# Optimization experiments

Hardware: AMD Instinct MI355X
Metric: run time of the kernel (lower is better)

The kernel has to match this reference:

```python
import jax, jax.numpy as jnp
import numpy as np

B, K, D, H = 4, 2048, 768, 12
HD = D // H
NEG = -1e30  # stands in for -inf in the additive mask


def setup_inputs() -> dict:
    key = jax.random.key(0)
    ks = jax.random.split(key, 11)
    s = 1.0 / np.sqrt(D)
    inp = {
        "x": jax.random.normal(ks[0], (B, K, D), jnp.float32),
        "is_context": jax.random.randint(ks[1], (B, K), 0, 2) > 0,
        "Wq": jax.random.normal(ks[2], (D, D), jnp.float32) * s,
        "bq": jax.random.normal(ks[3], (D,), jnp.float32) * 0.01,
        "Wk": jax.random.normal(ks[4], (D, D), jnp.float32) * s,
        "bk": jax.random.normal(ks[5], (D,), jnp.float32) * 0.01,
        "Wv": jax.random.normal(ks[6], (D, D), jnp.float32) * s,
        "bv": jax.random.normal(ks[7], (D,), jnp.float32) * 0.01,
        "Wo": jax.random.normal(ks[8], (D, D), jnp.float32) * s,
        "bo": jax.random.normal(ks[9], (D,), jnp.float32) * 0.01,
    }
    return inp


def reference(x, is_context, Wq, bq, Wk, bk, Wv, bv, Wo, bo):
    b, k_len, d = x.shape
    scale = 1.0 / jnp.sqrt(jnp.asarray(HD, x.dtype))
    # torch nn.Linear: y = x @ W.T + b
    q = (x @ Wq.T + bq).reshape(b, k_len, H, HD).transpose(0, 2, 1, 3)  # [B,H,K,hd]
    kk = (x @ Wk.T + bk).reshape(b, k_len, H, HD).transpose(0, 2, 1, 3)
    v = (x @ Wv.T + bv).reshape(b, k_len, H, HD).transpose(0, 2, 1, 3)

    ctx = is_context  # [B,K] bool
    # allowed[b,i,j]: context rows attend only to context cols; target rows attend to all
    allowed = (ctx[:, :, None] & ctx[:, None, :]) | (~ctx)[:, :, None]  # [B,K,K]

    scores = jnp.einsum("bhqd,bhkd->bhqk", q, kk) * scale  # [B,H,K,K]
    scores = jnp.where(allowed[:, None, :, :], scores, NEG)
    attn = jax.nn.softmax(scores, axis=-1)
    out = jnp.einsum("bhqk,bhkd->bhqd", attn, v)  # [B,H,K,hd]
    out = out.transpose(0, 2, 1, 3).reshape(b, k_len, d)
    return out @ Wo.T + bo
```

## Files before the change

### kernel.cpp

```cpp
#include <hip/hip_runtime.h>
#include <hip/hip_bf16.h>

constexpr int BATCH = 4;
constexpr int SEQ   = 2048;
constexpr int DIM   = 768;
constexpr int NH    = 12;
constexpr int HDIM  = 64;

typedef __attribute__((ext_vector_type(8))) short bf16x8;
typedef __attribute__((ext_vector_type(4))) float f32x4;
typedef __attribute__((ext_vector_type(4))) short s16x4;

__device__ inline short f2bf(float f) {
    union { float f; unsigned u; } v; v.f = f;
    unsigned r = (v.u + 0x7fff + ((v.u >> 16) & 1)) >> 16;
    return (short)r;
}

__device__ inline unsigned pack_bf16x2(float a, float b) {
    union { __hip_bfloat162 h; unsigned u; } c;
    c.h = __float22bfloat162_rn(make_float2(a, b));
    return c.u;
}

__device__ inline float fast_exp2(float x) {
#if __has_builtin(__builtin_amdgcn_exp2f)
    return __builtin_amdgcn_exp2f(x);
#else
    return __expf(x * 0.6931471805599453f);
#endif
}

__device__ inline void gld16(const short* g, short* l) {
    __builtin_amdgcn_global_load_lds(
        (const __attribute__((address_space(1))) void*)g,
        (__attribute__((address_space(3))) void*)l, 16, 0, 0);
}

__device__ inline bool ctx_at(const void* p, bool isU8, int idx) {
    return isU8 ? (((const unsigned char*)p)[idx] != 0)
                : (((const int*)p)[idx] != 0);
}

__global__ __launch_bounds__(256) void prep_kernel(
    const float* __restrict__ x,  const float* __restrict__ Wq,
    const float* __restrict__ Wk, const float* __restrict__ Wv,
    const float* __restrict__ Wo,
    short* __restrict__ xb,  short* __restrict__ Wqb,
    short* __restrict__ Wkb, short* __restrict__ Wvb,
    short* __restrict__ Wob,
    const unsigned char* __restrict__ ctxm, int ctxbytes, int* __restrict__ flag) {
    const int blk = blockIdx.x;
    constexpr int XBLK = (BATCH * SEQ * DIM / 4) / 256;
    constexpr int WBLK = (DIM * DIM / 4) / 256;

    if (blk == XBLK + 4 * WBLK) {
        __shared__ int cnt;
        if (threadIdx.x == 0) cnt = 0;
        __syncthreads();
        int local = 0;
        for (int i = threadIdx.x; i < ctxbytes; i += 256)
            if ((i & 3) != 0 && ctxm[i] != 0) local++;
        atomicAdd(&cnt, local);
        __syncthreads();
        if (threadIdx.x == 0) *flag = (cnt > 0) ? 1 : 0;
        return;
    }

    const float* src; short* dst; int i;
    if (blk < XBLK) {
        src = x; dst = xb;
        i = blk * 256 + threadIdx.x;
    } else {
        const int r = blk - XBLK;
        const int w = r / WBLK;
        src = (w == 0) ? Wq : (w == 1) ? Wk : (w == 2) ? Wv : Wo;
        dst = (w == 0) ? Wqb : (w == 1) ? Wkb : (w == 2) ? Wvb : Wob;
        i = (r - w * WBLK) * 256 + threadIdx.x;
    }
    float4 v = ((const float4*)src)[i];
    s16x4 o;
    o.x = f2bf(v.x); o.y = f2bf(v.y); o.z = f2bf(v.z); o.w = f2bf(v.w);
    ((s16x4*)dst)[i] = o;
}

template <bool BF16OUT>
__global__ __launch_bounds__(256) void gemm_mfma(
    const short* __restrict__ A,
    const short* __restrict__ W0, const float* __restrict__ bias0, void* __restrict__ C0,
    const short* __restrict__ W1, const float* __restrict__ bias1, void* __restrict__ C1,
    const short* __restrict__ W2, const float* __restrict__ bias2, void* __restrict__ C2,
    float scale0) {
    constexpr int N  = DIM;
    constexpr int Kd = DIM;

    const short* W; const float* bias; void* C; float scale;
    if (blockIdx.z == 0)      { W = W0; bias = bias0; C = C0; scale = scale0; }
    else if (blockIdx.z == 1) { W = W1; bias = bias1; C = C1; scale = 1.f; }
    else                      { W = W2; bias = bias2; C = C2; scale = 1.f; }

    const int tid  = threadIdx.x;
    const int wave = tid >> 6;
    const int lane = tid & 63;
    const int quad = lane >> 4;
    const int l16  = lane & 15;
    const int wm   = wave & 1;
    const int wn   = wave >> 1;
    const int m0   = blockIdx.y * 128;
    const int n0   = blockIdx.x * 128;

    __shared__ short As[128 * 32];
    __shared__ short Bs[128 * 32];

    const int srow = tid >> 2;
    const int skq  = tid & 3;
    const short* Ag = A + (size_t)(m0 + srow) * Kd + skq * 8;
    const short* Wg = W + (size_t)(n0 + srow) * Kd + skq * 8;
    short* AsP = As + srow * 32 + skq * 8;
    short* BsP = Bs + srow * 32 + skq * 8;

    f32x4 acc[4][4] = {};

    for (int kt = 0; kt < Kd; kt += 32) {
        __syncthreads();
        gld16(Ag + kt,                AsP);
        gld16(Ag + kt + 64 * Kd,      AsP + 64 * 32);
        gld16(Wg + kt,                BsP);
        gld16(Wg + kt + 64 * Kd,      BsP + 64 * 32);
        __syncthreads();

        bf16x8 af[4], bfr[4];
#pragma unroll
        for (int mt = 0; mt < 4; ++mt)
            af[mt] = *(const bf16x8*)&As[(wm * 64 + mt * 16 + l16) * 32 + quad * 8];
#pragma unroll
        for (int nt = 0; nt < 4; ++nt)
            bfr[nt] = *(const bf16x8*)&Bs[(wn * 64 + nt * 16 + l16) * 32 + quad * 8];
#pragma unroll
        for (int mt = 0; mt < 4; ++mt)
#pragma unroll
            for (int nt = 0; nt < 4; ++nt)
                acc[mt][nt] = __builtin_amdgcn_mfma_f32_16x16x32_bf16(
                    af[mt], bfr[nt], acc[mt][nt], 0, 0, 0);
    }

    float bv[4];
#pragma unroll
    for (int nt = 0; nt < 4; ++nt) bv[nt] = bias[n0 + wn * 64 + nt * 16 + l16];

#pragma unroll
    for (int mt = 0; mt < 4; ++mt)
#pragma unroll
        for (int nt = 0; nt < 4; ++nt)
#pragma unroll
            for (int reg = 0; reg < 4; ++reg) {
                const int m = m0 + wm * 64 + mt * 16 + quad * 4 + reg;
                const int n = n0 + wn * 64 + nt * 16 + l16;
                const float v = (acc[mt][nt][reg] + bv[nt]) * scale;
                if (BF16OUT) ((short*)C)[(size_t)m * N + n] = f2bf(v);
                else         ((float*)C)[(size_t)m * N + n] = v;
            }
}

__global__ __launch_bounds__(256) void vtrans_kernel(
    const short* __restrict__ Vb, short* __restrict__ Vtg) {
    const int b  = blockIdx.z;
    const int h  = blockIdx.y;
    const int k0 = blockIdx.x * 64;
    const int kl = threadIdx.x & 15;
    const int d0 = (threadIdx.x >> 4) * 4;

    s16x4 vr[4];
#pragma unroll
    for (int g = 0; g < 4; ++g)
        vr[g] = *(const s16x4*)(Vb + (size_t)(b * SEQ + k0 + g * 16 + kl) * DIM
                                + h * HDIM + d0);
#pragma unroll
    for (int i = 0; i < 4; ++i) {
        s16x4 w = {vr[0][i], vr[1][i], vr[2][i], vr[3][i]};
        *(s16x4*)(Vtg + (size_t)((b * NH + h) * HDIM + d0 + i) * SEQ + k0 + 4 * kl) = w;
    }
}

__global__ __launch_bounds__(256, 3) void attn_mfma6(
    const short* __restrict__ Qb, const short* __restrict__ Kb,
    const short* __restrict__ Vtg, const void* __restrict__ ctxp,
    const int* __restrict__ flagp, short* __restrict__ Ob) {
    const int b    = blockIdx.z;
    const int h    = blockIdx.y;
    const int q0   = blockIdx.x * 128;
    const int tid  = threadIdx.x;
    const int wave = tid >> 6;
    const int lane = tid & 63;
    const int quad = lane >> 4;
    const int l16  = lane & 15;
    const bool isU8 = (*flagp != 0);

    __shared__ short Ks[2][64 * 64];
    __shared__ short Vs[2][64 * 64];
    __shared__ short Ps[4][32 * 64];

    short* Pw = Ps[wave];

    const short* Kg = Kb + (size_t)b * SEQ * DIM + h * HDIM;
    const short* Vg = Vtg + (size_t)(b * NH + h) * HDIM * SEQ;

    const int r0 = tid >> 3;
    const int j0 = (tid & 7) ^ (r0 & 7);
    const int sw = l16 & 7;

    bf16x8 qf[2][2];
#pragma unroll
    for (int rg = 0; rg < 2; ++rg) {
        const short* qp = Qb + (size_t)(b * SEQ + q0 + wave * 32 + rg * 16 + l16) * DIM
                        + h * HDIM + quad * 8;
        qf[rg][0] = *(const bf16x8*)qp;
        qf[rg][1] = *(const bf16x8*)(qp + 32);
    }

    unsigned nmb[2][4];
#pragma unroll
    for (int rg = 0; rg < 2; ++rg)
#pragma unroll
        for (int reg = 0; reg < 4; ++reg)
            nmb[rg][reg] = ctx_at(ctxp, isU8,
                b * SEQ + q0 + wave * 32 + rg * 16 + quad * 4 + reg) ? 0u : 0xFFFFFFFFu;

    bf16x8 ones;
#pragma unroll
    for (int i = 0; i < 8; ++i) ones[i] = (short)0x3F80;

    f32x4 accl[2] = {};
    f32x4 acc[2][4] = {};

    {
        gld16(Kg + (size_t)r0 * DIM + j0 * 8,        &Ks[0][tid * 8]);
        gld16(Kg + (size_t)(r0 + 32) * DIM + j0 * 8, &Ks[0][(tid + 256) * 8]);
        gld16(Vg + (size_t)r0 * SEQ + j0 * 8,        &Vs[0][tid * 8]);
        gld16(Vg + (size_t)(r0 + 32) * SEQ + j0 * 8, &Vs[0][(tid + 256) * 8]);
    }

    constexpr int NT = SEQ / 64;
    for (int t = 0; t < NT; ++t) {
        const int k0  = t * 64;
        const int cur = t & 1;

        __syncthreads();

        if (t + 1 < NT) {
            const int kn  = k0 + 64;
            const int nxt = cur ^ 1;
            gld16(Kg + (size_t)(kn + r0) * DIM + j0 * 8,        &Ks[nxt][tid * 8]);
            gld16(Kg + (size_t)(kn + r0 + 32) * DIM + j0 * 8,   &Ks[nxt][(tid + 256) * 8]);
            gld16(Vg + (size_t)r0 * SEQ + kn + j0 * 8,          &Vs[nxt][tid * 8]);
            gld16(Vg + (size_t)(r0 + 32) * SEQ + kn + j0 * 8,   &Vs[nxt][(tid + 256) * 8]);
        }

        const short* BK = Ks[cur];
        const short* BV = Vs[cur];

        const unsigned long long kmask =
            __ballot(ctx_at(ctxp, isU8, b * SEQ + k0 + lane));
        unsigned km2[2];
#pragma unroll
        for (int gp = 0; gp < 2; ++gp) {
            const unsigned lo = (unsigned)((kmask >> (gp * 32 + l16)) & 1ull);
            const unsigned hi = (unsigned)((kmask >> (gp * 32 + 16 + l16)) & 1ull);
            km2[gp] = (lo ? 0x0000FFFFu : 0u) | (hi ? 0xFFFF0000u : 0u);
        }

        f32x4 s4[2][4] = {};
#pragma unroll
        for (int ks = 0; ks < 2; ++ks) {
            bf16x8 kf[4];
#pragma unroll
            for (int g = 0; g < 4; ++g)
                kf[g] = *(const bf16x8*)
                    &BK[(g * 16 + l16) * 64 + (((ks * 4 + quad) ^ sw)) * 8];
#pragma unroll
            for (int g = 0; g < 4; ++g) {
                s4[0][g] = __builtin_amdgcn_mfma_f32_16x16x32_bf16(qf[0][ks], kf[g], s4[0][g], 0, 0, 0);
                s4[1][g] = __builtin_amdgcn_mfma_f32_16x16x32_bf16(qf[1][ks], kf[g], s4[1][g], 0, 0, 0);
            }
        }

#pragma unroll
        for (int rg = 0; rg < 2; ++rg)
#pragma unroll
            for (int reg = 0; reg < 4; ++reg) {
                const float p0 = fast_exp2(s4[rg][0][reg]);
                const float p1 = fast_exp2(s4[rg][1][reg]);
                const float p2 = fast_exp2(s4[rg][2][reg]);
                const float p3 = fast_exp2(s4[rg][3][reg]);
                uint2 w;
                w.x = pack_bf16x2(p0, p1) & (nmb[rg][reg] | km2[0]);
                w.y = pack_bf16x2(p2, p3) & (nmb[rg][reg] | km2[1]);
                const int row = rg * 16 + quad * 4 + reg;
                const int pos = (l16 >> 1) ^ (row & 7);
                *(uint2*)&Pw[row * 64 + pos * 8 + (l16 & 1) * 4] = w;
            }

#pragma unroll
        for (int ks = 0; ks < 2; ++ks) {
            const int rpos = (ks * 4 + quad) ^ sw;
            bf16x8 pf0 = *(const bf16x8*)&Pw[l16 * 64 + rpos * 8];
            bf16x8 pf1 = *(const bf16x8*)&Pw[(16 + l16) * 64 + rpos * 8];
            accl[0] = __builtin_amdgcn_mfma_f32_16x16x32_bf16(pf0, ones, accl[0], 0, 0, 0);
            accl[1] = __builtin_amdgcn_mfma_f32_16x16x32_bf16(pf1, ones, accl[1], 0, 0, 0);
#pragma unroll
            for (int dt = 0; dt < 4; ++dt) {
                bf16x8 vf = *(const bf16x8*)
                    &BV[(dt * 16 + l16) * 64 + (((ks * 4 + quad) ^ sw)) * 8];
                acc[0][dt] = __builtin_amdgcn_mfma_f32_16x16x32_bf16(pf0, vf, acc[0][dt], 0, 0, 0);
                acc[1][dt] = __builtin_amdgcn_mfma_f32_16x16x32_bf16(pf1, vf, acc[1][dt], 0, 0, 0);
            }
        }
    }

    float inv[2][4];
#pragma unroll
    for (int rg = 0; rg < 2; ++rg)
#pragma unroll
        for (int reg = 0; reg < 4; ++reg)
            inv[rg][reg] = 1.f / accl[rg][reg];

#pragma unroll
    for (int rg = 0; rg < 2; ++rg)
#pragma unroll
        for (int dt = 0; dt < 4; ++dt)
#pragma unroll
            for (int reg = 0; reg < 4; ++reg) {
                const int q = q0 + wave * 32 + rg * 16 + quad * 4 + reg;
                Ob[(size_t)(b * SEQ + q) * DIM + h * HDIM + dt * 16 + l16] =
                    f2bf(acc[rg][dt][reg] * inv[rg][reg]);
            }
}

extern "C" void kernel_launch(void* const* d_in, const int* in_sizes, int n_in,
                              void* d_out, int out_size, void* d_ws, size_t ws_size,
                              hipStream_t stream) {
    const float* x   = (const float*)d_in[0];
    const void*  ctx = d_in[1];
    const float* Wq  = (const float*)d_in[2];
    const float* bq  = (const float*)d_in[3];
    const float* Wk  = (const float*)d_in[4];
    const float* bk  = (const float*)d_in[5];
    const float* Wv  = (const float*)d_in[6];
    const float* bv  = (const float*)d_in[7];
    const float* Wo  = (const float*)d_in[8];
    const float* bo  = (const float*)d_in[9];
    float* out = (float*)d_out;

    char* ws = (char*)d_ws;
    int* flag = (int*)ws;
    const size_t bufbf = (size_t)BATCH * SEQ * DIM * sizeof(short);
    const size_t wbuf  = (size_t)DIM * DIM * sizeof(short);
    short* xb  = (short*)(ws + 256);
    short* Qb  = (short*)(ws + 256 + bufbf);
    short* Kb  = (short*)(ws + 256 + 2 * bufbf);
    short* Vb  = (short*)(ws + 256 + 3 * bufbf);
    short* Ab  = (short*)(ws + 256 + 4 * bufbf);
    short* Vtg = (short*)(ws + 256 + 5 * bufbf);
    short* Wqb = (short*)(ws + 256 + 6 * bufbf);
    short* Wkb = (short*)(ws + 256 + 6 * bufbf + wbuf);
    short* Wvb = (short*)(ws + 256 + 6 * bufbf + 2 * wbuf);
    short* Wob = (short*)(ws + 256 + 6 * bufbf + 3 * wbuf);

    constexpr int XBLK = (BATCH * SEQ * DIM / 4) / 256;
    constexpr int WBLK = (DIM * DIM / 4) / 256;
    prep_kernel<<<XBLK + 4 * WBLK + 1, 256, 0, stream>>>(
        x, Wq, Wk, Wv, Wo, xb, Wqb, Wkb, Wvb, Wob,
        (const unsigned char*)ctx, BATCH * SEQ, flag);

    dim3 gQKV(DIM / 128, (BATCH * SEQ) / 128, 3);
    gemm_mfma<true><<<gQKV, 256, 0, stream>>>(
        xb, Wqb, bq, Qb, Wkb, bk, Kb, Wvb, bv, Vb, 0.125f * 1.4426950408889634f);

    dim3 gVt(SEQ / 64, NH, BATCH);
    vtrans_kernel<<<gVt, 256, 0, stream>>>(Vb, Vtg);

    dim3 gAttn(SEQ / 128, NH, BATCH);
    attn_mfma6<<<gAttn, 256, 0, stream>>>(Qb, Kb, Vtg, ctx, flag, Ab);

    dim3 gOut(DIM / 128, (BATCH * SEQ) / 128, 1);
    gemm_mfma<false><<<gOut, 256, 0, stream>>>(
        Ab, Wob, bo, out, Wob, bo, out, Wob, bo, out, 1.f);
}
```

Baseline: 259.6 us.

## Keep softmax probabilities in registers via transposed QK^T and permuted V layout

Computes S^T by swapping the MFMA operands so each lane holds probabilities along the key dimension. It then builds the PV A-operand fragments in registers using a cross-half lane shuffle instead of a round trip through per-wave shared memory. To keep the V operand consistent with the new key ordering, the V-transpose kernel now writes keys in a matching permuted order. It also raises wave priority around the MFMA blocks. This removes the shared-memory writes and reads of P and frees that LDS, at the cost of shuffles and extra index arithmetic.

```diff
diff --git a/kernel.cpp b/kernel.cpp
--- a/kernel.cpp
+++ b/kernel.cpp
@@ -167,22 +167,27 @@
     const int b  = blockIdx.z;
     const int h  = blockIdx.y;
     const int k0 = blockIdx.x * 64;
-    const int kl = threadIdx.x & 15;
+    const int pw = threadIdx.x & 15;
     const int d0 = (threadIdx.x >> 4) * 4;
 
+    const int ks = pw >> 3;
+    const int w  = pw & 7;
+    const int q  = w >> 1;
+    const int kbase = ks * 32 + ((w & 1) ? (16 + (q ^ 2) * 4) : (q * 4));
+
     s16x4 vr[4];
 #pragma unroll
     for (int g = 0; g < 4; ++g)
-        vr[g] = *(const s16x4*)(Vb + (size_t)(b * SEQ + k0 + g * 16 + kl) * DIM
+        vr[g] = *(const s16x4*)(Vb + (size_t)(b * SEQ + k0 + kbase + g) * DIM
                                 + h * HDIM + d0);
 #pragma unroll
     for (int i = 0; i < 4; ++i) {
-        s16x4 w = {vr[0][i], vr[1][i], vr[2][i], vr[3][i]};
-        *(s16x4*)(Vtg + (size_t)((b * NH + h) * HDIM + d0 + i) * SEQ + k0 + 4 * kl) = w;
-    }
-}
-
-__global__ __launch_bounds__(256, 3) void attn_mfma6(
+        s16x4 o = {vr[0][i], vr[1][i], vr[2][i], vr[3][i]};
+        *(s16x4*)(Vtg + (size_t)((b * NH + h) * HDIM + d0 + i) * SEQ + k0 + 4 * pw) = o;
+    }
+}
+
+__global__ __launch_bounds__(256, 3) void attn_mfma7(
     const short* __restrict__ Qb, const short* __restrict__ Kb,
     const short* __restrict__ Vtg, const void* __restrict__ ctxp,
     const int* __restrict__ flagp, short* __restrict__ Ob) {
@@ -198,9 +203,6 @@
 
     __shared__ short Ks[2][64 * 64];
     __shared__ short Vs[2][64 * 64];
-    __shared__ short Ps[4][32 * 64];
-
-    short* Pw = Ps[wave];
 
     const short* Kg = Kb + (size_t)b * SEQ * DIM + h * HDIM;
     const short* Vg = Vtg + (size_t)(b * NH + h) * HDIM * SEQ;
@@ -218,13 +220,11 @@
         qf[rg][1] = *(const bf16x8*)(qp + 32);
     }
 
-    unsigned nmb[2][4];
+    unsigned nmb[2];
 #pragma unroll
     for (int rg = 0; rg < 2; ++rg)
-#pragma unroll
-        for (int reg = 0; reg < 4; ++reg)
-            nmb[rg][reg] = ctx_at(ctxp, isU8,
-                b * SEQ + q0 + wave * 32 + rg * 16 + quad * 4 + reg) ? 0u : 0xFFFFFFFFu;
+        nmb[rg] = ctx_at(ctxp, isU8,
+            b * SEQ + q0 + wave * 32 + rg * 16 + l16) ? 0u : 0xFFFFFFFFu;
 
     bf16x8 ones;
 #pragma unroll
@@ -261,15 +261,9 @@
 
         const unsigned long long kmask =
             __ballot(ctx_at(ctxp, isU8, b * SEQ + k0 + lane));
-        unsigned km2[2];
-#pragma unroll
-        for (int gp = 0; gp < 2; ++gp) {
-            const unsigned lo = (unsigned)((kmask >> (gp * 32 + l16)) & 1ull);
-            const unsigned hi = (unsigned)((kmask >> (gp * 32 + 16 + l16)) & 1ull);
-            km2[gp] = (lo ? 0x0000FFFFu : 0u) | (hi ? 0xFFFF0000u : 0u);
-        }
-
-        f32x4 s4[2][4] = {};
+
+        f32x4 s4[4][2] = {};
+        __builtin_amdgcn_s_setprio(1);
 #pragma unroll
         for (int ks = 0; ks < 2; ++ks) {
             bf16x8 kf[4];
@@ -279,42 +273,64 @@
                     &BK[(g * 16 + l16) * 64 + (((ks * 4 + quad) ^ sw)) * 8];
 #pragma unroll
             for (int g = 0; g < 4; ++g) {
-                s4[0][g] = __builtin_amdgcn_mfma_f32_16x16x32_bf16(qf[0][ks], kf[g], s4[0][g], 0, 0, 0);
-                s4[1][g] = __builtin_amdgcn_mfma_f32_16x16x32_bf16(qf[1][ks], kf[g], s4[1][g], 0, 0, 0);
+                s4[g][0] = __builtin_amdgcn_mfma_f32_16x16x32_bf16(kf[g], qf[0][ks], s4[g][0], 0, 0, 0);
+                s4[g][1] = __builtin_amdgcn_mfma_f32_16x16x32_bf16(kf[g], qf[1][ks], s4[g][1], 0, 0, 0);
             }
         }
-
-#pragma unroll
-        for (int rg = 0; rg < 2; ++rg)
-#pragma unroll
-            for (int reg = 0; reg < 4; ++reg) {
-                const float p0 = fast_exp2(s4[rg][0][reg]);
-                const float p1 = fast_exp2(s4[rg][1][reg]);
-                const float p2 = fast_exp2(s4[rg][2][reg]);
-                const float p3 = fast_exp2(s4[rg][3][reg]);
-                uint2 w;
-                w.x = pack_bf16x2(p0, p1) & (nmb[rg][reg] | km2[0]);
-                w.y = pack_bf16x2(p2, p3) & (nmb[rg][reg] | km2[1]);
-                const int row = rg * 16 + quad * 4 + reg;
-                const int pos = (l16 >> 1) ^ (row & 7);
-                *(uint2*)&Pw[row * 64 + pos * 8 + (l16 & 1) * 4] = w;
-            }
-
+        __builtin_amdgcn_s_setprio(0);
+
+        unsigned mw[2][4];
+#pragma unroll
+        for (int ks = 0; ks < 2; ++ks)
+#pragma unroll
+            for (int w = 0; w < 4; ++w) {
+                const int base = 32 * ks + ((w >> 1) & 1) * 16 + quad * 4 + (w & 1) * 2;
+                const unsigned two = (unsigned)(kmask >> base) & 3u;
+                mw[ks][w] = ((two & 1u) ? 0x0000FFFFu : 0u) |
+                            ((two & 2u) ? 0xFFFF0000u : 0u);
+            }
+
+        bf16x8 pa[2][2];
+#pragma unroll
+        for (int rg = 0; rg < 2; ++rg) {
+            const unsigned nm = nmb[rg];
+#pragma unroll
+            for (int ks = 0; ks < 2; ++ks) {
+                const int g0 = 2 * ks, g1 = 2 * ks + 1;
+                const float e0 = fast_exp2(s4[g0][rg][0]);
+                const float e1 = fast_exp2(s4[g0][rg][1]);
+                const float e2 = fast_exp2(s4[g0][rg][2]);
+                const float e3 = fast_exp2(s4[g0][rg][3]);
+                const float e4 = fast_exp2(s4[g1][rg][0]);
+                const float e5 = fast_exp2(s4[g1][rg][1]);
+                const float e6 = fast_exp2(s4[g1][rg][2]);
+                const float e7 = fast_exp2(s4[g1][rg][3]);
+                const unsigned wA0 = pack_bf16x2(e0, e1) & (nm | mw[ks][0]);
+                const unsigned wA1 = pack_bf16x2(e2, e3) & (nm | mw[ks][1]);
+                const unsigned wB0 = pack_bf16x2(e4, e5) & (nm | mw[ks][2]);
+                const unsigned wB1 = pack_bf16x2(e6, e7) & (nm | mw[ks][3]);
+                const unsigned pB0 = (unsigned)__shfl((int)wB0, lane ^ 32);
+                const unsigned pB1 = (unsigned)__shfl((int)wB1, lane ^ 32);
+                union { bf16x8 v; unsigned u[4]; } tb;
+                tb.u[0] = wA0; tb.u[1] = wA1; tb.u[2] = pB0; tb.u[3] = pB1;
+                pa[rg][ks] = tb.v;
+            }
+        }
+
+        __builtin_amdgcn_s_setprio(1);
 #pragma unroll
         for (int ks = 0; ks < 2; ++ks) {
-            const int rpos = (ks * 4 + quad) ^ sw;
-            bf16x8 pf0 = *(const bf16x8*)&Pw[l16 * 64 + rpos * 8];
-            bf16x8 pf1 = *(const bf16x8*)&Pw[(16 + l16) * 64 + rpos * 8];
-            accl[0] = __builtin_amdgcn_mfma_f32_16x16x32_bf16(pf0, ones, accl[0], 0, 0, 0);
-            accl[1] = __builtin_amdgcn_mfma_f32_16x16x32_bf16(pf1, ones, accl[1], 0, 0, 0);
+            accl[0] = __builtin_amdgcn_mfma_f32_16x16x32_bf16(pa[0][ks], ones, accl[0], 0, 0, 0);
+            accl[1] = __builtin_amdgcn_mfma_f32_16x16x32_bf16(pa[1][ks], ones, accl[1], 0, 0, 0);
 #pragma unroll
             for (int dt = 0; dt < 4; ++dt) {
                 bf16x8 vf = *(const bf16x8*)
                     &BV[(dt * 16 + l16) * 64 + (((ks * 4 + quad) ^ sw)) * 8];
-                acc[0][dt] = __builtin_amdgcn_mfma_f32_16x16x32_bf16(pf0, vf, acc[0][dt], 0, 0, 0);
-                acc[1][dt] = __builtin_amdgcn_mfma_f32_16x16x32_bf16(pf1, vf, acc[1][dt], 0, 0, 0);
+                acc[0][dt] = __builtin_amdgcn_mfma_f32_16x16x32_bf16(pa[0][ks], vf, acc[0][dt], 0, 0, 0);
+                acc[1][dt] = __builtin_amdgcn_mfma_f32_16x16x32_bf16(pa[1][ks], vf, acc[1][dt], 0, 0, 0);
             }
         }
+        __builtin_amdgcn_s_setprio(0);
     }
 
     float inv[2][4];
@@ -380,7 +396,7 @@
     vtrans_kernel<<<gVt, 256, 0, stream>>>(Vb, Vtg);
 
     dim3 gAttn(SEQ / 128, NH, BATCH);
-    attn_mfma6<<<gAttn, 256, 0, stream>>>(Qb, Kb, Vtg, ctx, flag, Ab);
+    attn_mfma7<<<gAttn, 256, 0, stream>>>(Qb, Kb, Vtg, ctx, flag, Ab);
 
     dim3 gOut(DIM / 128, (BATCH * SEQ) / 128, 1);
     gemm_mfma<false><<<gOut, 256, 0, stream>>>(
```

Result: no change. 259.8 us (+0.1%).
